# Optimization experiments

Hardware: AMD Instinct MI355X
Metric: run time of the kernel (lower is better)

The kernel has to match this reference:

```python
import jax, jax.numpy as jnp
import numpy as np

V, C, E, L, M = 100000, 420000, 1260000, 3, 64
FV = FC = 3
ED = 2


def _gru(x, h, wih, whh, bih, bhh):
    # PyTorch GRUCell semantics. x: [N, in], h: [N, H], wih: [3H, in], whh: [3H, H]
    gi = x @ wih.T + bih
    gh = h @ whh.T + bhh
    H = h.shape[-1]
    r = jax.nn.sigmoid(gi[:, :H] + gh[:, :H])
    z = jax.nn.sigmoid(gi[:, H:2 * H] + gh[:, H:2 * H])
    n = jnp.tanh(gi[:, 2 * H:] + r * gh[:, 2 * H:])
    return (1.0 - z) * n + z * h


def setup_inputs() -> dict:
    key = jax.random.key(0)
    ks = iter(jax.random.split(key, 40))
    f = lambda shape, s=0.1: jax.random.normal(next(ks), shape, jnp.float32) * s
    inp = {
        'var_features': jax.random.normal(next(ks), (V, FV), jnp.float32),
        'clause_features': jax.random.normal(next(ks), (C, FC), jnp.float32),
        'edge_features': jax.random.uniform(next(ks), (E, ED), dtype=jnp.float32),
        'v2c_w1': f((L, M, FV + ED)), 'v2c_b1': f((L, M)),
        'v2c_w2': f((L, M, M)), 'v2c_b2': f((L, M)),
        'c2v_w1': f((L, M, FC + ED)), 'c2v_b1': f((L, M)),
        'c2v_w2': f((L, M, M)), 'c2v_b2': f((L, M)),
        'var_gru_wih': f((L, 3 * FV, M)), 'var_gru_whh': f((L, 3 * FV, FV)),
        'var_gru_bih': f((L, 3 * FV)), 'var_gru_bhh': f((L, 3 * FV)),
        'cls_gru_wih': f((L, 3 * FC, M)), 'cls_gru_whh': f((L, 3 * FC, FC)),
        'cls_gru_bih': f((L, 3 * FC)), 'cls_gru_bhh': f((L, 3 * FC)),
        'att_w1': f((L, M, FC)), 'att_b1': f((L, M)),
        'att_w2': f((L, 1, M)), 'att_b2': f((L, 1)),
        'var_idx': jax.random.randint(next(ks), (E,), 0, V),
        'clause_idx': jax.random.randint(next(ks), (E,), 0, C),
    }
    return inp


def reference(var_features, clause_features, edge_features,
              v2c_w1, v2c_b1, v2c_w2, v2c_b2,
              c2v_w1, c2v_b1, c2v_w2, c2v_b2,
              var_gru_wih, var_gru_whh, var_gru_bih, var_gru_bhh,
              cls_gru_wih, cls_gru_whh, cls_gru_bih, cls_gru_bhh,
              att_w1, att_b1, att_w2, att_b2,
              var_idx, clause_idx):
    vf, cf = var_features, clause_features
    for l in range(L):  # fixed small number of message-passing steps
        # var -> clause: gather, edge MLP, attention-weight, scatter-add
        v2c_in = jnp.concatenate([vf[var_idx], edge_features], axis=1)  # [E, FV+ED]
        m = jnp.maximum(v2c_in @ v2c_w1[l].T + v2c_b1[l], 0.0) @ v2c_w2[l].T + v2c_b2[l]  # [E, M]
        att = (jnp.tanh(cf @ att_w1[l].T + att_b1[l]) @ att_w2[l].T + att_b2[l])[:, 0]  # [C]
        att = jax.nn.softmax(att, axis=0)
        m = m * att[clause_idx][:, None]
        cmsg = jax.ops.segment_sum(m, clause_idx, num_segments=C)  # [C, M]
        cf_new = _gru(cmsg, cf, cls_gru_wih[l], cls_gru_whh[l], cls_gru_bih[l], cls_gru_bhh[l])
        # clause -> var uses OLD clause features (matches torch forward ordering)
        c2v_in = jnp.concatenate([cf[clause_idx], edge_features], axis=1)  # [E, FC+ED]
        mv = jnp.maximum(c2v_in @ c2v_w1[l].T + c2v_b1[l], 0.0) @ c2v_w2[l].T + c2v_b2[l]  # [E, M]
        vmsg = jax.ops.segment_sum(mv, var_idx, num_segments=V)  # [V, M]
        vf = _gru(vmsg, vf, var_gru_wih[l], var_gru_whh[l], var_gru_bih[l], var_gru_bhh[l])
        cf = cf_new
    return jnp.concatenate([vf, cf], axis=0)  # [V+C, 3]
```

## Files before the change

kernel.cpp:

```cpp
#include <hip/hip_runtime.h>
#include <hip/hip_fp16.h>
#include <math.h>

#define V_N 100000
#define C_N 420000
#define E_N 1260000
#define L_N 3

__device__ __forceinline__ float fsig(float x) {
    return 1.0f / (1.0f + __expf(-x));
}
__device__ __forceinline__ float ftanh(float x) {
    x = fminf(fmaxf(x, -15.0f), 15.0f);
    float t = __expf(2.0f * x);
    return (t - 1.0f) / (t + 1.0f);
}

__global__ void k_prep(const float* __restrict__ v2c_w1, const float* __restrict__ v2c_b1,
                       const float* __restrict__ v2c_w2, const float* __restrict__ v2c_b2,
                       const float* __restrict__ c2v_w1, const float* __restrict__ c2v_b1,
                       const float* __restrict__ c2v_w2, const float* __restrict__ c2v_b2,
                       const float* __restrict__ cls_wih, const float* __restrict__ var_wih,
                       float* __restrict__ prep) {
    int t = blockIdx.x * blockDim.x + threadIdx.x;
    if (t >= 6 * 1040) return;
    int s = t / 1040, r = t % 1040;
    int side = s / 3, l = s % 3;
    const float* w1  = (side ? c2v_w1 : v2c_w1) + l * 320;
    const float* b1  = (side ? c2v_b1 : v2c_b1) + l * 64;
    const float* W2  = (side ? c2v_w2 : v2c_w2) + l * 4096;
    const float* b2  = (side ? c2v_b2 : v2c_b2) + l * 64;
    const float* wih = (side ? var_wih : cls_wih) + l * 576;
    float v = 0.0f;
    if (r < 1024) {
        int j = r >> 4, q = r & 15;
        if (q < 5) v = w1[j * 5 + q];
        else if (q == 5) v = b1[j];
        else if (q < 15) {
            int k = q - 6; float a = 0.0f;
            for (int o = 0; o < 64; ++o) a += wih[k * 64 + o] * W2[o * 64 + j];
            v = a;
        }
    } else if (r < 1033) {
        int k = r - 1024; float a = 0.0f;
        for (int o = 0; o < 64; ++o) a += wih[k * 64 + o] * b2[o];
        v = a;
    }
    prep[t] = v;
}

__global__ __launch_bounds__(256) void k_count(const int* __restrict__ ci, const int* __restrict__ vi,
                                               int* __restrict__ cntC, int* __restrict__ cntV) {
    int e = blockIdx.x * 256 + threadIdx.x;
    if (e >= E_N) return;
    atomicAdd(&cntC[ci[e]], 1);
    atomicAdd(&cntV[vi[e]], 1);
}

__global__ __launch_bounds__(256) void k_scan1(const int* __restrict__ cnt, int N,
                                               int* __restrict__ bsum) {
    int b = blockIdx.x, t = threadIdx.x;
    int base = b * 1024 + t * 4;
    int s = 0;
    #pragma unroll
    for (int q = 0; q < 4; ++q) { int i = base + q; if (i < N) s += cnt[i]; }
    __shared__ int sh[256];
    sh[t] = s; __syncthreads();
    for (int d = 128; d; d >>= 1) { if (t < d) sh[t] += sh[t + d]; __syncthreads(); }
    if (t == 0) bsum[b] = sh[0];
}

__global__ __launch_bounds__(512) void k_scan2(int* __restrict__ bsum, int nb,
                                               int* __restrict__ rowN) {
    __shared__ int sh[512];
    int t = threadIdx.x;
    int v = (t < nb) ? bsum[t] : 0;
    sh[t] = v; __syncthreads();
    for (int d = 1; d < 512; d <<= 1) {
        int add = (t >= d) ? sh[t - d] : 0;
        __syncthreads();
        sh[t] += add;
        __syncthreads();
    }
    if (t < nb) bsum[t] = sh[t] - v;
    if (t == nb - 1) *rowN = sh[t];
}

__global__ __launch_bounds__(256) void k_scan3(const int* __restrict__ cnt, int N,
                                               const int* __restrict__ bsum,
                                               int* __restrict__ row, int* __restrict__ curs) {
    int b = blockIdx.x, t = threadIdx.x;
    int base = b * 1024 + t * 4;
    int v[4], local[4];
    #pragma unroll
    for (int q = 0; q < 4; ++q) { int i = base + q; v[q] = (i < N) ? cnt[i] : 0; }
    local[0] = 0; local[1] = v[0]; local[2] = v[0] + v[1]; local[3] = v[0] + v[1] + v[2];
    int mysum = local[3] + v[3];
    __shared__ int sh[256];
    sh[t] = mysum; __syncthreads();
    for (int d = 1; d < 256; d <<= 1) {
        int add = (t >= d) ? sh[t - d] : 0;
        __syncthreads();
        sh[t] += add;
        __syncthreads();
    }
    int excl = sh[t] - mysum + bsum[b];
    #pragma unroll
    for (int q = 0; q < 4; ++q) {
        int i = base + q;
        if (i < N) { int p = excl + local[q]; row[i] = p; curs[i] = p; }
    }
}

__global__ __launch_bounds__(256) void k_fill(const int* __restrict__ ci, const int* __restrict__ vi,
                                              int* __restrict__ cursC, int* __restrict__ cursV,
                                              int* __restrict__ invC, int* __restrict__ invV) {
    int e = blockIdx.x * 256 + threadIdx.x;
    if (e >= E_N) return;
    invC[e] = atomicAdd(&cursC[ci[e]], 1);
    invV[e] = atomicAdd(&cursV[vi[e]], 1);
}

__global__ __launch_bounds__(256) void k_att(const float* __restrict__ cf,
                                             const float* __restrict__ aw1,
                                             const float* __restrict__ ab1,
                                             const float* __restrict__ aw2,
                                             const float* __restrict__ ab2,
                                             float* __restrict__ logits,
                                             float* __restrict__ pmax) {
    int c = blockIdx.x * blockDim.x + threadIdx.x;
    float logit = -1e30f;
    if (c < C_N) {
        float h0 = cf[c * 3], h1 = cf[c * 3 + 1], h2 = cf[c * 3 + 2];
        float acc = ab2[0];
        #pragma unroll
        for (int k = 0; k < 64; ++k) {
            float tv = ftanh(aw1[k * 3] * h0 + aw1[k * 3 + 1] * h1 +
                             aw1[k * 3 + 2] * h2 + ab1[k]);
            acc += aw2[k] * tv;
        }
        logits[c] = acc;
        logit = acc;
    }
    float m = logit;
    #pragma unroll
    for (int off = 32; off; off >>= 1) m = fmaxf(m, __shfl_xor(m, off));
    __shared__ float smax[4];
    int lane = threadIdx.x & 63, wid = threadIdx.x >> 6;
    if (lane == 0) smax[wid] = m;
    __syncthreads();
    if (threadIdx.x == 0)
        pmax[blockIdx.x] = fmaxf(fmaxf(smax[0], smax[1]), fmaxf(smax[2], smax[3]));
}

__global__ __launch_bounds__(256) void k_sum(const float* __restrict__ logits,
                                             const float* __restrict__ pmax, int npmax,
                                             float* __restrict__ Spart) {
    __shared__ float sh[4];
    float m = -1e30f;
    for (int i = threadIdx.x; i < npmax; i += 256) m = fmaxf(m, pmax[i]);
    #pragma unroll
    for (int off = 32; off; off >>= 1) m = fmaxf(m, __shfl_xor(m, off));
    int lane = threadIdx.x & 63, wid = threadIdx.x >> 6;
    if (lane == 0) sh[wid] = m;
    __syncthreads();
    float mm = fmaxf(fmaxf(sh[0], sh[1]), fmaxf(sh[2], sh[3]));
    __syncthreads();
    int c = blockIdx.x * 256 + threadIdx.x;
    float e = (c < C_N) ? __expf(logits[c] - mm) : 0.0f;
    #pragma unroll
    for (int off = 32; off; off >>= 1) e += __shfl_xor(e, off);
    if (lane == 0) sh[wid] = e;
    __syncthreads();
    if (threadIdx.x == 0) Spart[blockIdx.x] = sh[0] + sh[1] + sh[2] + sh[3];
}

__global__ __launch_bounds__(256) void k_red(const float* __restrict__ Spart,
                                             const float* __restrict__ pmax, int n,
                                             float* __restrict__ Sg) {
    __shared__ float sh[8];
    float s = 0.0f, m = -1e30f;
    for (int i = threadIdx.x; i < n; i += 256) { s += Spart[i]; m = fmaxf(m, pmax[i]); }
    #pragma unroll
    for (int off = 32; off; off >>= 1) { s += __shfl_xor(s, off); m = fmaxf(m, __shfl_xor(m, off)); }
    int lane = threadIdx.x & 63, wid = threadIdx.x >> 6;
    if (lane == 0) { sh[wid] = s; sh[4 + wid] = m; }
    __syncthreads();
    if (threadIdx.x == 0) {
        Sg[0] = sh[0] + sh[1] + sh[2] + sh[3];
        Sg[1] = fmaxf(fmaxf(sh[4], sh[5]), fmaxf(sh[6], sh[7]));
    }
}

__global__ __launch_bounds__(256) void k_edge(const float* __restrict__ feat,
                                              const float* __restrict__ ef,
                                              const int* __restrict__ gidx,
                                              const int* __restrict__ inv,
                                              const float* __restrict__ prep,
                                              uint2* __restrict__ umsg) {
    __shared__ float W[1040];
    for (int i = threadIdx.x; i < 1040; i += 256) W[i] = prep[i];
    __syncthreads();
    int e = blockIdx.x * 256 + threadIdx.x;
    if (e >= E_N) return;
    int g = gidx[e];
    float x0 = feat[g * 3], x1 = feat[g * 3 + 1], x2 = feat[g * 3 + 2];
    float2 efv = *(const float2*)(ef + 2 * (size_t)e);
    float u[9];
    #pragma unroll
    for (int k = 0; k < 9; ++k) u[k] = 0.0f;
    for (int j = 0; j < 64; ++j) {
        const float* wj = &W[j * 16];
        float h = wj[0] * x0 + wj[1] * x1 + wj[2] * x2 + wj[3] * efv.x + wj[4] * efv.y + wj[5];
        h = fmaxf(h, 0.0f);
        #pragma unroll
        for (int k = 0; k < 9; ++k) u[k] += wj[6 + k] * h;
    }
    union { __half h[12]; uint2 q[3]; } pk;
    #pragma unroll
    for (int k = 0; k < 9; ++k) pk.h[k] = __float2half(u[k]);
    pk.h[9] = pk.h[10] = pk.h[11] = __float2half(0.0f);
    size_t pos = (size_t)inv[e] * 3;
    umsg[pos] = pk.q[0]; umsg[pos + 1] = pk.q[1]; umsg[pos + 2] = pk.q[2];
}

template <bool ATT>
__global__ __launch_bounds__(256) void k_node(const uint2* __restrict__ umsg,
                                              const int* __restrict__ row,
                                              const float* __restrict__ hin,
                                              const float* __restrict__ logits,
                                              const float* __restrict__ Sg,
                                              const float* __restrict__ c2,
                                              const float* __restrict__ whh,
                                              const float* __restrict__ bih,
                                              const float* __restrict__ bhh,
                                              float* __restrict__ hout, int N) {
    int i = blockIdx.x * 256 + threadIdx.x;
    if (i >= N) return;
    int p0 = row[i], p1 = row[i + 1];
    float u[9];
    #pragma unroll
    for (int k = 0; k < 9; ++k) u[k] = 0.0f;
    for (int p = p0; p < p1; ++p) {
        union { __half h[12]; uint2 q[3]; } pk;
        const uint2* r = umsg + (size_t)p * 3;
        pk.q[0] = r[0]; pk.q[1] = r[1]; pk.q[2] = r[2];
        #pragma unroll
        for (int k = 0; k < 9; ++k) u[k] += __half2float(pk.h[k]);
    }
    float cnt = (float)(p1 - p0);
    float scale = 1.0f;
    if (ATT) scale = __expf(logits[i] - Sg[1]) / Sg[0];
    float h0 = hin[i * 3], h1 = hin[i * 3 + 1], h2 = hin[i * 3 + 2];
    float gi[9], gh[9];
    #pragma unroll
    for (int k = 0; k < 9; ++k) gi[k] = scale * (u[k] + cnt * c2[k]) + bih[k];
    #pragma unroll
    for (int k = 0; k < 9; ++k)
        gh[k] = whh[k * 3] * h0 + whh[k * 3 + 1] * h1 + whh[k * 3 + 2] * h2 + bhh[k];
    float r0 = fsig(gi[0] + gh[0]), r1 = fsig(gi[1] + gh[1]), r2 = fsig(gi[2] + gh[2]);
    float z0 = fsig(gi[3] + gh[3]), z1 = fsig(gi[4] + gh[4]), z2 = fsig(gi[5] + gh[5]);
    float n0 = ftanh(gi[6] + r0 * gh[6]);
    float n1 = ftanh(gi[7] + r1 * gh[7]);
    float n2 = ftanh(gi[8] + r2 * gh[8]);
    hout[i * 3 + 0] = (1.0f - z0) * n0 + z0 * h0;
    hout[i * 3 + 1] = (1.0f - z1) * n1 + z1 * h1;
    hout[i * 3 + 2] = (1.0f - z2) * n2 + z2 * h2;
}

extern "C" void kernel_launch(void* const* d_in, const int* in_sizes, int n_in,
                              void* d_out, int out_size, void* d_ws, size_t ws_size,
                              hipStream_t stream) {
    const float* vf0     = (const float*)d_in[0];
    const float* cf0     = (const float*)d_in[1];
    const float* ef      = (const float*)d_in[2];
    const float* v2c_w1  = (const float*)d_in[3];
    const float* v2c_b1  = (const float*)d_in[4];
    const float* v2c_w2  = (const float*)d_in[5];
    const float* v2c_b2  = (const float*)d_in[6];
    const float* c2v_w1  = (const float*)d_in[7];
    const float* c2v_b1  = (const float*)d_in[8];
    const float* c2v_w2  = (const float*)d_in[9];
    const float* c2v_b2  = (const float*)d_in[10];
    const float* var_wih = (const float*)d_in[11];
    const float* var_whh = (const float*)d_in[12];
    const float* var_bih = (const float*)d_in[13];
    const float* var_bhh = (const float*)d_in[14];
    const float* cls_wih = (const float*)d_in[15];
    const float* cls_whh = (const float*)d_in[16];
    const float* cls_bih = (const float*)d_in[17];
    const float* cls_bhh = (const float*)d_in[18];
    const float* att_w1  = (const float*)d_in[19];
    const float* att_b1  = (const float*)d_in[20];
    const float* att_w2  = (const float*)d_in[21];
    const float* att_b2  = (const float*)d_in[22];
    const int*   var_idx = (const int*)d_in[23];
    const int*   cls_idx = (const int*)d_in[24];
    float* dout = (float*)d_out;

    char* w = (char*)d_ws;
    auto alloc = [&](size_t bytes) { char* p = w; w += (bytes + 255) & ~(size_t)255; return p; };
    int*   rowC   = (int*)alloc((C_N + 1) * 4);
    int*   rowV   = (int*)alloc((V_N + 1) * 4);
    int*   cursC  = (int*)alloc((size_t)C_N * 4);
    int*   cursV  = (int*)alloc((size_t)V_N * 4);
    int*   invC   = (int*)alloc((size_t)E_N * 4);
    int*   invV   = (int*)alloc((size_t)E_N * 4);
    int*   bsum   = (int*)alloc(512 * 4);
    float* logits = (float*)alloc((size_t)C_N * 4);
    float* pmax   = (float*)alloc(2048 * 4);
    float* Spart  = (float*)alloc(2048 * 4);
    float* Sg     = (float*)alloc(2 * 4);
    float* prep   = (float*)alloc(6 * 1040 * 4);
    uint2* umsg   = (uint2*)alloc((size_t)E_N * 3 * 8);
    float* vfA    = (float*)alloc((size_t)V_N * 3 * 4);
    float* vfB    = (float*)alloc((size_t)V_N * 3 * 4);
    float* cfA    = (float*)alloc((size_t)C_N * 3 * 4);
    float* cfB    = (float*)alloc((size_t)C_N * 3 * 4);

    const int nE = (E_N + 255) / 256;
    const int nC = (C_N + 255) / 256;
    const int nV = (V_N + 255) / 256;
    const int nbC = (C_N + 1023) / 1024;
    const int nbV = (V_N + 1023) / 1024;

    k_prep<<<(6 * 1040 + 255) / 256, 256, 0, stream>>>(
        v2c_w1, v2c_b1, v2c_w2, v2c_b2, c2v_w1, c2v_b1, c2v_w2, c2v_b2,
        cls_wih, var_wih, prep);

    hipMemsetAsync(cursC, 0, (size_t)C_N * 4, stream);
    hipMemsetAsync(cursV, 0, (size_t)V_N * 4, stream);
    k_count<<<nE, 256, 0, stream>>>(cls_idx, var_idx, cursC, cursV);
    k_scan1<<<nbC, 256, 0, stream>>>(cursC, C_N, bsum);
    k_scan2<<<1, 512, 0, stream>>>(bsum, nbC, rowC + C_N);
    k_scan3<<<nbC, 256, 0, stream>>>(cursC, C_N, bsum, rowC, cursC);
    k_scan1<<<nbV, 256, 0, stream>>>(cursV, V_N, bsum);
    k_scan2<<<1, 512, 0, stream>>>(bsum, nbV, rowV + V_N);
    k_scan3<<<nbV, 256, 0, stream>>>(cursV, V_N, bsum, rowV, cursV);
    k_fill<<<nE, 256, 0, stream>>>(cls_idx, var_idx, cursC, cursV, invC, invV);

    const float* vf_cur = vf0;
    const float* cf_cur = cf0;
    for (int l = 0; l < L_N; ++l) {
        float* vf_next = (l == 0) ? vfA : (l == 1) ? vfB : dout;
        float* cf_next = (l == 0) ? cfA : (l == 1) ? cfB : (dout + (size_t)V_N * 3);

        k_att<<<nC, 256, 0, stream>>>(cf_cur, att_w1 + l * 192, att_b1 + l * 64,
                                      att_w2 + l * 64, att_b2 + l, logits, pmax);
        k_sum<<<nC, 256, 0, stream>>>(logits, pmax, nC, Spart);
        k_red<<<1, 256, 0, stream>>>(Spart, pmax, nC, Sg);

        k_edge<<<nE, 256, 0, stream>>>(vf_cur, ef, var_idx, invC,
                                       prep + (0 * 3 + l) * 1040, umsg);
        k_node<true><<<nC, 256, 0, stream>>>(umsg, rowC, cf_cur, logits, Sg,
                                             prep + (0 * 3 + l) * 1040 + 1024,
                                             cls_whh + l * 27, cls_bih + l * 9,
                                             cls_bhh + l * 9, cf_next, C_N);

        k_edge<<<nE, 256, 0, stream>>>(cf_cur, ef, cls_idx, invV,
                                       prep + (1 * 3 + l) * 1040, umsg);
        k_node<false><<<nV, 256, 0, stream>>>(umsg, rowV, vf_cur, logits, Sg,
                                              prep + (1 * 3 + l) * 1040 + 1024,
                                              var_whh + l * 27, var_bih + l * 9,
                                              var_bhh + l * 9, vf_next, V_N);

        vf_cur = vf_next;
        cf_cur = cf_next;
    }
}
```

Baseline: 984.5 us.

## Merge CSR build into count-rank pass and fuse softmax reduction via atomics

Each edge's rank within its segment is now recorded during the counting atomics, which removes the separate fill pass and its second set of atomics. Edge kernels compute the destination slot as row offset plus rank. The clause and variable scans are batched into shared launches, and the final softmax-sum reduction kernel is replaced by a float atomic add into the global sum. This cuts kernel launches and one full edge pass. In exchange, edge kernels do an extra indirect load per edge, and the order of the float atomic accumulation is nondeterministic.

```diff
diff --git a/kernel.cpp b/kernel.cpp
--- a/kernel.cpp
+++ b/kernel.cpp
@@ -49,29 +49,38 @@
     prep[t] = v;
 }
 
-__global__ __launch_bounds__(256) void k_count(const int* __restrict__ ci, const int* __restrict__ vi,
-                                               int* __restrict__ cntC, int* __restrict__ cntV) {
+__global__ __launch_bounds__(256) void k_countrank(const int* __restrict__ ci,
+                                                   const int* __restrict__ vi,
+                                                   int* __restrict__ cntC, int* __restrict__ cntV,
+                                                   int* __restrict__ rankC, int* __restrict__ rankV) {
     int e = blockIdx.x * 256 + threadIdx.x;
     if (e >= E_N) return;
-    atomicAdd(&cntC[ci[e]], 1);
-    atomicAdd(&cntV[vi[e]], 1);
-}
-
-__global__ __launch_bounds__(256) void k_scan1(const int* __restrict__ cnt, int N,
-                                               int* __restrict__ bsum) {
+    rankC[e] = atomicAdd(&cntC[ci[e]], 1);
+    rankV[e] = atomicAdd(&cntV[vi[e]], 1);
+}
+
+__global__ __launch_bounds__(256) void k_scanA(const int* __restrict__ cntC,
+                                               const int* __restrict__ cntV, int nbC,
+                                               int* __restrict__ bsumC, int* __restrict__ bsumV) {
     int b = blockIdx.x, t = threadIdx.x;
-    int base = b * 1024 + t * 4;
+    const int* cnt; int N; int* bs; int bb;
+    if (b < nbC) { cnt = cntC; N = C_N; bs = bsumC; bb = b; }
+    else         { cnt = cntV; N = V_N; bs = bsumV; bb = b - nbC; }
+    int base = bb * 1024 + t * 4;
     int s = 0;
     #pragma unroll
     for (int q = 0; q < 4; ++q) { int i = base + q; if (i < N) s += cnt[i]; }
     __shared__ int sh[256];
     sh[t] = s; __syncthreads();
     for (int d = 128; d; d >>= 1) { if (t < d) sh[t] += sh[t + d]; __syncthreads(); }
-    if (t == 0) bsum[b] = sh[0];
-}
-
-__global__ __launch_bounds__(512) void k_scan2(int* __restrict__ bsum, int nb,
-                                               int* __restrict__ rowN) {
+    if (t == 0) bs[bb] = sh[0];
+}
+
+__global__ __launch_bounds__(512) void k_scanB(int* __restrict__ bsumC, int nbC, int* __restrict__ totC,
+                                               int* __restrict__ bsumV, int nbV, int* __restrict__ totV) {
+    int* bsum = blockIdx.x ? bsumV : bsumC;
+    int nb    = blockIdx.x ? nbV : nbC;
+    int* tot  = blockIdx.x ? totV : totC;
     __shared__ int sh[512];
     int t = threadIdx.x;
     int v = (t < nb) ? bsum[t] : 0;
@@ -83,14 +92,19 @@
         __syncthreads();
     }
     if (t < nb) bsum[t] = sh[t] - v;
-    if (t == nb - 1) *rowN = sh[t];
-}
-
-__global__ __launch_bounds__(256) void k_scan3(const int* __restrict__ cnt, int N,
-                                               const int* __restrict__ bsum,
-                                               int* __restrict__ row, int* __restrict__ curs) {
+    if (t == nb - 1) *tot = sh[t];
+}
+
+__global__ __launch_bounds__(256) void k_scanC(const int* __restrict__ cntC,
+                                               const int* __restrict__ cntV, int nbC,
+                                               const int* __restrict__ bsumC,
+                                               const int* __restrict__ bsumV,
+                                               int* __restrict__ rowC, int* __restrict__ rowV) {
     int b = blockIdx.x, t = threadIdx.x;
-    int base = b * 1024 + t * 4;
+    const int* cnt; int N; const int* bs; int* row; int bb;
+    if (b < nbC) { cnt = cntC; N = C_N; bs = bsumC; row = rowC; bb = b; }
+    else         { cnt = cntV; N = V_N; bs = bsumV; row = rowV; bb = b - nbC; }
+    int base = bb * 1024 + t * 4;
     int v[4], local[4];
     #pragma unroll
     for (int q = 0; q < 4; ++q) { int i = base + q; v[q] = (i < N) ? cnt[i] : 0; }
@@ -104,21 +118,12 @@
         sh[t] += add;
         __syncthreads();
     }
-    int excl = sh[t] - mysum + bsum[b];
+    int excl = sh[t] - mysum + bs[bb];
     #pragma unroll
     for (int q = 0; q < 4; ++q) {
         int i = base + q;
-        if (i < N) { int p = excl + local[q]; row[i] = p; curs[i] = p; }
-    }
-}
-
-__global__ __launch_bounds__(256) void k_fill(const int* __restrict__ ci, const int* __restrict__ vi,
-                                              int* __restrict__ cursC, int* __restrict__ cursV,
-                                              int* __restrict__ invC, int* __restrict__ invV) {
-    int e = blockIdx.x * 256 + threadIdx.x;
-    if (e >= E_N) return;
-    invC[e] = atomicAdd(&cursC[ci[e]], 1);
-    invV[e] = atomicAdd(&cursV[vi[e]], 1);
+        if (i < N) row[i] = excl + local[q];
+    }
 }
 
 __global__ __launch_bounds__(256) void k_att(const float* __restrict__ cf,
@@ -127,7 +132,9 @@
                                              const float* __restrict__ aw2,
                                              const float* __restrict__ ab2,
                                              float* __restrict__ logits,
-                                             float* __restrict__ pmax) {
+                                             float* __restrict__ pmax,
+                                             float* __restrict__ Sg) {
+    if (blockIdx.x == 0 && threadIdx.x == 0) Sg[0] = 0.0f;
     int c = blockIdx.x * blockDim.x + threadIdx.x;
     float logit = -1e30f;
     if (c < C_N) {
@@ -155,7 +162,7 @@
 
 __global__ __launch_bounds__(256) void k_sum(const float* __restrict__ logits,
                                              const float* __restrict__ pmax, int npmax,
-                                             float* __restrict__ Spart) {
+                                             float* __restrict__ Sg) {
     __shared__ float sh[4];
     float m = -1e30f;
     for (int i = threadIdx.x; i < npmax; i += 256) m = fmaxf(m, pmax[i]);
@@ -172,30 +179,18 @@
     for (int off = 32; off; off >>= 1) e += __shfl_xor(e, off);
     if (lane == 0) sh[wid] = e;
     __syncthreads();
-    if (threadIdx.x == 0) Spart[blockIdx.x] = sh[0] + sh[1] + sh[2] + sh[3];
-}
-
-__global__ __launch_bounds__(256) void k_red(const float* __restrict__ Spart,
-                                             const float* __restrict__ pmax, int n,
-                                             float* __restrict__ Sg) {
-    __shared__ float sh[8];
-    float s = 0.0f, m = -1e30f;
-    for (int i = threadIdx.x; i < n; i += 256) { s += Spart[i]; m = fmaxf(m, pmax[i]); }
-    #pragma unroll
-    for (int off = 32; off; off >>= 1) { s += __shfl_xor(s, off); m = fmaxf(m, __shfl_xor(m, off)); }
-    int lane = threadIdx.x & 63, wid = threadIdx.x >> 6;
-    if (lane == 0) { sh[wid] = s; sh[4 + wid] = m; }
-    __syncthreads();
     if (threadIdx.x == 0) {
-        Sg[0] = sh[0] + sh[1] + sh[2] + sh[3];
-        Sg[1] = fmaxf(fmaxf(sh[4], sh[5]), fmaxf(sh[6], sh[7]));
+        unsafeAtomicAdd(&Sg[0], sh[0] + sh[1] + sh[2] + sh[3]);
+        if (blockIdx.x == 0) Sg[1] = mm;
     }
 }
 
 __global__ __launch_bounds__(256) void k_edge(const float* __restrict__ feat,
                                               const float* __restrict__ ef,
                                               const int* __restrict__ gidx,
-                                              const int* __restrict__ inv,
+                                              const int* __restrict__ didx,
+                                              const int* __restrict__ row,
+                                              const int* __restrict__ rank,
                                               const float* __restrict__ prep,
                                               uint2* __restrict__ umsg) {
     __shared__ float W[1040];
@@ -204,6 +199,7 @@
     int e = blockIdx.x * 256 + threadIdx.x;
     if (e >= E_N) return;
     int g = gidx[e];
+    int pos = row[didx[e]] + rank[e];
     float x0 = feat[g * 3], x1 = feat[g * 3 + 1], x2 = feat[g * 3 + 2];
     float2 efv = *(const float2*)(ef + 2 * (size_t)e);
     float u[9];
@@ -220,8 +216,8 @@
     #pragma unroll
     for (int k = 0; k < 9; ++k) pk.h[k] = __float2half(u[k]);
     pk.h[9] = pk.h[10] = pk.h[11] = __float2half(0.0f);
-    size_t pos = (size_t)inv[e] * 3;
-    umsg[pos] = pk.q[0]; umsg[pos + 1] = pk.q[1]; umsg[pos + 2] = pk.q[2];
+    size_t p = (size_t)pos * 3;
+    umsg[p] = pk.q[0]; umsg[p + 1] = pk.q[1]; umsg[p + 2] = pk.q[2];
 }
 
 template <bool ATT>
@@ -302,15 +298,16 @@
     auto alloc = [&](size_t bytes) { char* p = w; w += (bytes + 255) & ~(size_t)255; return p; };
     int*   rowC   = (int*)alloc((C_N + 1) * 4);
     int*   rowV   = (int*)alloc((V_N + 1) * 4);
-    int*   cursC  = (int*)alloc((size_t)C_N * 4);
-    int*   cursV  = (int*)alloc((size_t)V_N * 4);
-    int*   invC   = (int*)alloc((size_t)E_N * 4);
-    int*   invV   = (int*)alloc((size_t)E_N * 4);
-    int*   bsum   = (int*)alloc(512 * 4);
+    int*   cntC   = (int*)alloc((size_t)C_N * 4);
+    int*   cntV   = (int*)alloc((size_t)V_N * 4);
+    char*  cntEnd = w;
+    int*   rankC  = (int*)alloc((size_t)E_N * 4);
+    int*   rankV  = (int*)alloc((size_t)E_N * 4);
+    int*   bsumC  = (int*)alloc(512 * 4);
+    int*   bsumV  = (int*)alloc(512 * 4);
     float* logits = (float*)alloc((size_t)C_N * 4);
     float* pmax   = (float*)alloc(2048 * 4);
-    float* Spart  = (float*)alloc(2048 * 4);
-    float* Sg     = (float*)alloc(2 * 4);
+    float* Sg     = (float*)alloc(64 * 4);
     float* prep   = (float*)alloc(6 * 1040 * 4);
     uint2* umsg   = (uint2*)alloc((size_t)E_N * 3 * 8);
     float* vfA    = (float*)alloc((size_t)V_N * 3 * 4);
@@ -318,9 +315,9 @@
     float* cfA    = (float*)alloc((size_t)C_N * 3 * 4);
     float* cfB    = (float*)alloc((size_t)C_N * 3 * 4);
 
-    const int nE = (E_N + 255) / 256;
-    const int nC = (C_N + 255) / 256;
-    const int nV = (V_N + 255) / 256;
+    const int nE  = (E_N + 255) / 256;
+    const int nC  = (C_N + 255) / 256;
+    const int nV  = (V_N + 255) / 256;
     const int nbC = (C_N + 1023) / 1024;
     const int nbV = (V_N + 1023) / 1024;
 
@@ -328,16 +325,11 @@
         v2c_w1, v2c_b1, v2c_w2, v2c_b2, c2v_w1, c2v_b1, c2v_w2, c2v_b2,
         cls_wih, var_wih, prep);
 
-    hipMemsetAsync(cursC, 0, (size_t)C_N * 4, stream);
-    hipMemsetAsync(cursV, 0, (size_t)V_N * 4, stream);
-    k_count<<<nE, 256, 0, stream>>>(cls_idx, var_idx, cursC, cursV);
-    k_scan1<<<nbC, 256, 0, stream>>>(cursC, C_N, bsum);
-    k_scan2<<<1, 512, 0, stream>>>(bsum, nbC, rowC + C_N);
-    k_scan3<<<nbC, 256, 0, stream>>>(cursC, C_N, bsum, rowC, cursC);
-    k_scan1<<<nbV, 256, 0, stream>>>(cursV, V_N, bsum);
-    k_scan2<<<1, 512, 0, stream>>>(bsum, nbV, rowV + V_N);
-    k_scan3<<<nbV, 256, 0, stream>>>(cursV, V_N, bsum, rowV, cursV);
-    k_fill<<<nE, 256, 0, stream>>>(cls_idx, var_idx, cursC, cursV, invC, invV);
+    hipMemsetAsync(cntC, 0, (size_t)(cntEnd - (char*)cntC), stream);
+    k_countrank<<<nE, 256, 0, stream>>>(cls_idx, var_idx, cntC, cntV, rankC, rankV);
+    k_scanA<<<nbC + nbV, 256, 0, stream>>>(cntC, cntV, nbC, bsumC, bsumV);
+    k_scanB<<<2, 512, 0, stream>>>(bsumC, nbC, rowC + C_N, bsumV, nbV, rowV + V_N);
+    k_scanC<<<nbC + nbV, 256, 0, stream>>>(cntC, cntV, nbC, bsumC, bsumV, rowC, rowV);
 
     const float* vf_cur = vf0;
     const float* cf_cur = cf0;
@@ -346,18 +338,17 @@
         float* cf_next = (l == 0) ? cfA : (l == 1) ? cfB : (dout + (size_t)V_N * 3);
 
         k_att<<<nC, 256, 0, stream>>>(cf_cur, att_w1 + l * 192, att_b1 + l * 64,
-                                      att_w2 + l * 64, att_b2 + l, logits, pmax);
-        k_sum<<<nC, 256, 0, stream>>>(logits, pmax, nC, Spart);
-        k_red<<<1, 256, 0, stream>>>(Spart, pmax, nC, Sg);
-
-        k_edge<<<nE, 256, 0, stream>>>(vf_cur, ef, var_idx, invC,
+                                      att_w2 + l * 64, att_b2 + l, logits, pmax, Sg);
+        k_sum<<<nC, 256, 0, stream>>>(logits, pmax, nC, Sg);
+
+        k_edge<<<nE, 256, 0, stream>>>(vf_cur, ef, var_idx, cls_idx, rowC, rankC,
                                        prep + (0 * 3 + l) * 1040, umsg);
         k_node<true><<<nC, 256, 0, stream>>>(umsg, rowC, cf_cur, logits, Sg,
                                              prep + (0 * 3 + l) * 1040 + 1024,
                                              cls_whh + l * 27, cls_bih + l * 9,
                                              cls_bhh + l * 9, cf_next, C_N);
 
-        k_edge<<<nE, 256, 0, stream>>>(cf_cur, ef, cls_idx, invV,
+        k_edge<<<nE, 256, 0, stream>>>(cf_cur, ef, cls_idx, var_idx, rowV, rankV,
                                        prep + (1 * 3 + l) * 1040, umsg);
         k_node<false><<<nV, 256, 0, stream>>>(umsg, rowV, vf_cur, logits, Sg,
                                               prep + (1 * 3 + l) * 1040 + 1024,
```

Measured after the change: 926.7 us. 5.9% less time.
